# Optimization experiments

Measured on AMD Instinct MI355X. Metric: run time of the kernel, lower is better.

## Reference

```python
import jax, jax.numpy as jnp
import numpy as np

B, T_EN, T_DE, D_EN, D_DE, UNITS = 16, 256, 256, 512, 512, 128


def setup_inputs() -> dict:
    key = jax.random.key(0)
    k1, k2, k3, k4, k5 = jax.random.split(key, 5)
    # glorot-uniform style scale for weights
    def glorot(k, shape):
        lim = np.sqrt(6.0 / (shape[0] + shape[1]))
        return jax.random.uniform(k, shape, jnp.float32, -lim, lim)
    return {
        "en_seq": jax.random.normal(k1, (B, T_EN, D_EN), jnp.float32),
        "de_seq": jax.random.normal(k2, (B, T_DE, D_DE), jnp.float32),
        "w_en": glorot(k3, (D_EN, UNITS)),
        "w_de": glorot(k4, (D_DE, UNITS)),
        "nu": glorot(k5, (UNITS, 1)),
    }


def reference(en_seq, de_seq, w_en, w_de, nu):
    # Additive (Bahdanau) time attention.
    # Original keras code builds the (de, en) cross product via K.repeat /
    # K.repeat_elements with de-major, en-minor ordering; equivalent to
    # broadcasting att_de over a new en axis and att_en over a new de axis.
    att_en = jnp.einsum("bie,eu->biu", en_seq, w_en)   # (B, T_en, U)
    att_de = jnp.einsum("bjd,du->bju", de_seq, w_de)   # (B, T_de, U)
    # co_m: (B, T_de, T_en, U) — the large broadcast intermediate
    co_m = jnp.tanh(att_de[:, :, None, :] + att_en[:, None, :, :])
    mu = jnp.einsum("bjiu,u->bji", co_m, nu[:, 0])      # (B, T_de, T_en)
    alphas = jax.nn.softmax(mu, axis=-1)                # softmax over encoder time
    sum_en = jnp.einsum("bji,bie->bje", alphas, en_seq)  # (B, T_de, D_en)
    return jnp.concatenate([de_seq, sum_en], axis=-1)    # (B, T_de, D_de + D_en)
```

## Files before the change

kernel.cpp:

```cpp
#include <hip/hip_runtime.h>
#include <hip/hip_bf16.h>

#define TANH_SCALE 2.8853900817779268f

__global__ __launch_bounds__(256) void proj_kernel(
        const float* __restrict__ en, const float* __restrict__ de,
        const float* __restrict__ w_en, const float* __restrict__ w_de,
        float* __restrict__ Een, float* __restrict__ Ede) {
    const float* X;
    const float* W;
    float* OUT;
    if (blockIdx.y == 0) { X = en; W = w_en; OUT = Een; }
    else                 { X = de; W = w_de; OUT = Ede; }

    __shared__ float xt[64][36];
    __shared__ float wsh[64][128];
    const int tid  = threadIdx.x;
    const int tr   = tid >> 5;
    const int tc   = tid & 31;
    const int row0 = blockIdx.x * 32;

    const int xs_r  = tid >> 4;
    const int xs_k4 = (tid & 15) * 4;
    float4 xr[2], wr[8];

    auto g_load = [&](int kt) {
#pragma unroll
        for (int s = 0; s < 2; ++s) {
            int r = xs_r + 16 * s;
            xr[s] = *reinterpret_cast<const float4*>(
                X + (size_t)(row0 + r) * 512 + kt + xs_k4);
        }
#pragma unroll
        for (int s = 0; s < 8; ++s) {
            int idx = tid + 256 * s;
            int k = idx >> 5, c4 = (idx & 31) * 4;
            wr[s] = *reinterpret_cast<const float4*>(
                W + (size_t)(kt + k) * 128 + c4);
        }
    };
    auto lds_store = [&]() {
        const int swz = ((xs_k4 >> 2) & 7) << 2;
#pragma unroll
        for (int s = 0; s < 2; ++s) {
            int r = (xs_r + 16 * s) ^ swz;
            xt[xs_k4 + 0][r] = xr[s].x;
            xt[xs_k4 + 1][r] = xr[s].y;
            xt[xs_k4 + 2][r] = xr[s].z;
            xt[xs_k4 + 3][r] = xr[s].w;
        }
#pragma unroll
        for (int s = 0; s < 8; ++s) {
            int idx = tid + 256 * s;
            int k = idx >> 5, c4 = (idx & 31) * 4;
            *reinterpret_cast<float4*>(&wsh[k][c4]) = wr[s];
        }
    };

    float acc[4][4] = {{0.f}};
    g_load(0);
    lds_store();
    __syncthreads();

    for (int kt = 0; kt < 512; kt += 64) {
        const bool has_next = (kt + 64) < 512;
        if (has_next) g_load(kt + 64);
#pragma unroll
        for (int k = 0; k < 64; ++k) {
            const int col = (tr * 4) ^ (((k >> 2) & 7) << 2);
            float4 xv = *reinterpret_cast<const float4*>(&xt[k][col]);
            float4 wv = *reinterpret_cast<const float4*>(&wsh[k][tc * 4]);
            acc[0][0] = fmaf(xv.x, wv.x, acc[0][0]);
            acc[0][1] = fmaf(xv.x, wv.y, acc[0][1]);
            acc[0][2] = fmaf(xv.x, wv.z, acc[0][2]);
            acc[0][3] = fmaf(xv.x, wv.w, acc[0][3]);
            acc[1][0] = fmaf(xv.y, wv.x, acc[1][0]);
            acc[1][1] = fmaf(xv.y, wv.y, acc[1][1]);
            acc[1][2] = fmaf(xv.y, wv.z, acc[1][2]);
            acc[1][3] = fmaf(xv.y, wv.w, acc[1][3]);
            acc[2][0] = fmaf(xv.z, wv.x, acc[2][0]);
            acc[2][1] = fmaf(xv.z, wv.y, acc[2][1]);
            acc[2][2] = fmaf(xv.z, wv.z, acc[2][2]);
            acc[2][3] = fmaf(xv.z, wv.w, acc[2][3]);
            acc[3][0] = fmaf(xv.w, wv.x, acc[3][0]);
            acc[3][1] = fmaf(xv.w, wv.y, acc[3][1]);
            acc[3][2] = fmaf(xv.w, wv.z, acc[3][2]);
            acc[3][3] = fmaf(xv.w, wv.w, acc[3][3]);
        }
        __syncthreads();
        if (has_next) {
            lds_store();
            __syncthreads();
        }
    }

#pragma unroll
    for (int r = 0; r < 4; ++r) {
        float4 o;
        o.x = __builtin_exp2f(-TANH_SCALE * acc[r][0]);
        o.y = __builtin_exp2f(-TANH_SCALE * acc[r][1]);
        o.z = __builtin_exp2f(-TANH_SCALE * acc[r][2]);
        o.w = __builtin_exp2f(-TANH_SCALE * acc[r][3]);
        *reinterpret_cast<float4*>(
            OUT + (size_t)(row0 + tr * 4 + r) * 128 + tc * 4) = o;
    }
}

__global__ __launch_bounds__(512, 4) void fused_attn_kernel(
        const float* __restrict__ Een, const float* __restrict__ Ede,
        const float* __restrict__ nu, const float* __restrict__ en,
        const float* __restrict__ de, float* __restrict__ out) {
    const int phys = blockIdx.x;
    const int lid  = (phys & 7) * 64 + (phys >> 3);
    const int b    = lid >> 5;
    const int j0   = (lid & 31) * 8;
    const int tid  = threadIdx.x;
    const int i    = tid & 255;
    const int uh   = tid >> 8;

    __shared__ float ede_sh[8][128];
    __shared__ float nu2_sh[128];
    __shared__ float nusum_sh[64];
    __shared__ float al[8][256];
    __shared__ float red[8][4];

    if (tid < 256)
        reinterpret_cast<float4*>(&ede_sh[0][0])[tid] =
            reinterpret_cast<const float4*>(Ede + ((size_t)b * 256 + j0) * 128)[tid];
    if (tid >= 256 && tid < 384) nu2_sh[tid - 256] = 2.0f * nu[tid - 256];
    if (tid >= 384 && tid < 448) {
        int t = tid - 384;
        nusum_sh[t] = 2.0f * (nu[2 * t] + nu[2 * t + 1]);
    }

    {
        const float4* dsrc =
            reinterpret_cast<const float4*>(de + ((size_t)b * 256 + j0) * 512);
#pragma unroll
        for (int t = 0; t < 2; ++t) {
            int idx = tid + 512 * t;
            int j = idx >> 7, c4 = idx & 127;
            reinterpret_cast<float4*>(out + (size_t)(b * 256 + j0 + j) * 1024)[c4] =
                dsrc[idx];
        }
    }
    __syncthreads();

    float s[4] = {0.0f, 0.0f, 0.0f, 0.0f};
    const float4* e4 =
        reinterpret_cast<const float4*>(Een + ((size_t)b * 256 + i) * 128);
    const float4* nu4 = reinterpret_cast<const float4*>(nu2_sh);
    const float4* cs4 = reinterpret_cast<const float4*>(nusum_sh);
    for (int q = 0; q < 16; ++q) {
        const float4 ea = e4[2 * q];
        const float4 eb = e4[2 * q + 1];
        const float4 na = nu4[2 * q];
        const float4 nb = nu4[2 * q + 1];
        const float4 cs = cs4[q];
#pragma unroll
        for (int jl = 0; jl < 4; ++jl) {
            const float* dr = &ede_sh[uh * 4 + jl][8 * q];
            const float4 da = *reinterpret_cast<const float4*>(dr);
            const float4 db = *reinterpret_cast<const float4*>(dr + 4);
            float e0, e1, den, num;
            e0 = ea.x * da.x; e1 = ea.y * da.y;
            den = 1.0f + e0; den = fmaf(den, e1, den);
            num = fmaf(na.x, e1, cs.x); num = fmaf(na.y, e0, num);
            s[jl] = fmaf(num, __builtin_amdgcn_rcpf(den), s[jl]);
            e0 = ea.z * da.z; e1 = ea.w * da.w;
            den = 1.0f + e0; den = fmaf(den, e1, den);
            num = fmaf(na.z, e1, cs.y); num = fmaf(na.w, e0, num);
            s[jl] = fmaf(num, __builtin_amdgcn_rcpf(den), s[jl]);
            e0 = eb.x * db.x; e1 = eb.y * db.y;
            den = 1.0f + e0; den = fmaf(den, e1, den);
            num = fmaf(nb.x, e1, cs.z); num = fmaf(nb.y, e0, num);
            s[jl] = fmaf(num, __builtin_amdgcn_rcpf(den), s[jl]);
            e0 = eb.z * db.z; e1 = eb.w * db.w;
            den = 1.0f + e0; den = fmaf(den, e1, den);
            num = fmaf(nb.z, e1, cs.w); num = fmaf(nb.w, e0, num);
            s[jl] = fmaf(num, __builtin_amdgcn_rcpf(den), s[jl]);
        }
    }

    float p[4];
#pragma unroll
    for (int jl = 0; jl < 4; ++jl) p[jl] = __expf(s[jl]);
    const int lane = tid & 63;
    const int w    = (tid >> 6) & 3;
#pragma unroll
    for (int jl = 0; jl < 4; ++jl) {
        float t = p[jl];
#pragma unroll
        for (int off = 32; off >= 1; off >>= 1) t += __shfl_xor(t, off);
        if (lane == 0) red[uh * 4 + jl][w] = t;
    }
    __syncthreads();
#pragma unroll
    for (int jl = 0; jl < 4; ++jl) {
        const int j = uh * 4 + jl;
        float T = red[j][0] + red[j][1] + red[j][2] + red[j][3];
        al[j][i] = p[jl] * __builtin_amdgcn_rcpf(T);
    }
    __syncthreads();

    float acc[8];
#pragma unroll
    for (int j = 0; j < 8; ++j) acc[j] = 0.0f;
    const float* enb = en + (size_t)b * 256 * 512;
    const int c = tid;
    for (int i0 = 0; i0 < 256; i0 += 4) {
        float a[8][4];
#pragma unroll
        for (int j = 0; j < 8; ++j) {
            float4 v = *reinterpret_cast<const float4*>(&al[j][i0]);
            a[j][0] = v.x; a[j][1] = v.y; a[j][2] = v.z; a[j][3] = v.w;
        }
#pragma unroll
        for (int ii = 0; ii < 4; ++ii) {
            float e0 = enb[(size_t)(i0 + ii) * 512 + c];
#pragma unroll
            for (int j = 0; j < 8; ++j)
                acc[j] = fmaf(a[j][ii], e0, acc[j]);
        }
    }
#pragma unroll
    for (int j = 0; j < 8; ++j) {
        size_t row = (size_t)(b * 256 + j0 + j);
        out[row * 1024 + 512 + c] = acc[j];
    }
}

extern "C" void kernel_launch(void* const* d_in, const int* in_sizes, int n_in,
                              void* d_out, int out_size, void* d_ws, size_t ws_size,
                              hipStream_t stream) {
    const float* en   = (const float*)d_in[0];
    const float* de   = (const float*)d_in[1];
    const float* w_en = (const float*)d_in[2];
    const float* w_de = (const float*)d_in[3];
    const float* nu   = (const float*)d_in[4];
    float* out = (float*)d_out;

    char* ws = (char*)d_ws;
    float* Een = (float*)(ws);
    float* Ede = (float*)(ws + (size_t)4096 * 128 * 4);

    proj_kernel<<<dim3(128, 2), 256, 0, stream>>>(en, de, w_en, w_de, Een, Ede);
    fused_attn_kernel<<<dim3(512), 512, 0, stream>>>(Een, Ede, nu, en, de, out);
}
```

Measured before the change: 160.9 us.

## Split-K projection GEMM with combine pass and transposed encoder layout with prefetch

The projection GEMM can now be split along K into two halves, which doubles the block count. A separate combine kernel adds the partials and applies the exp2 transform, but only when the workspace is large enough. The encoder projection is written in a transposed, u-pair-major layout so that threads in the attention kernel read consecutive i values as coalesced float2 loads. The attention loop also register-prefetches the next group of encoder values. The trade-off is an extra kernel launch and extra partial-sum traffic in exchange for more parallelism in the small projection and better load coalescing in the main kernel.

```diff
diff --git a/kernel.cpp b/kernel.cpp
--- a/kernel.cpp
+++ b/kernel.cpp
@@ -3,40 +3,25 @@
 
 #define TANH_SCALE 2.8853900817779268f
 
-__global__ __launch_bounds__(256) void proj_kernel(
-        const float* __restrict__ en, const float* __restrict__ de,
-        const float* __restrict__ w_en, const float* __restrict__ w_de,
-        float* __restrict__ Een, float* __restrict__ Ede) {
-    const float* X;
-    const float* W;
-    float* OUT;
-    if (blockIdx.y == 0) { X = en; W = w_en; OUT = Een; }
-    else                 { X = de; W = w_de; OUT = Ede; }
-
-    __shared__ float xt[64][36];
-    __shared__ float wsh[64][128];
-    const int tid  = threadIdx.x;
-    const int tr   = tid >> 5;
-    const int tc   = tid & 31;
-    const int row0 = blockIdx.x * 32;
-
+
+__device__ __forceinline__ void gemm_tile_32x128(
+        const float* __restrict__ X, const float* __restrict__ W,
+        int row0, int k0, int k1, int tid, float acc[4][4],
+        float (*xt)[36], float (*wsh)[128]) {
     const int xs_r  = tid >> 4;
     const int xs_k4 = (tid & 15) * 4;
     float4 xr[2], wr[8];
 
     auto g_load = [&](int kt) {
 #pragma unroll
-        for (int s = 0; s < 2; ++s) {
-            int r = xs_r + 16 * s;
+        for (int s = 0; s < 2; ++s)
             xr[s] = *reinterpret_cast<const float4*>(
-                X + (size_t)(row0 + r) * 512 + kt + xs_k4);
-        }
+                X + (size_t)(row0 + xs_r + 16 * s) * 512 + kt + xs_k4);
 #pragma unroll
         for (int s = 0; s < 8; ++s) {
             int idx = tid + 256 * s;
-            int k = idx >> 5, c4 = (idx & 31) * 4;
             wr[s] = *reinterpret_cast<const float4*>(
-                W + (size_t)(kt + k) * 128 + c4);
+                W + (size_t)(kt + (idx >> 5)) * 128 + (idx & 31) * 4);
         }
     };
     auto lds_store = [&]() {
@@ -52,18 +37,16 @@
 #pragma unroll
         for (int s = 0; s < 8; ++s) {
             int idx = tid + 256 * s;
-            int k = idx >> 5, c4 = (idx & 31) * 4;
-            *reinterpret_cast<float4*>(&wsh[k][c4]) = wr[s];
+            *reinterpret_cast<float4*>(&wsh[idx >> 5][(idx & 31) * 4]) = wr[s];
         }
     };
 
-    float acc[4][4] = {{0.f}};
-    g_load(0);
+    const int tr = tid >> 5, tc = tid & 31;
+    g_load(k0);
     lds_store();
     __syncthreads();
-
-    for (int kt = 0; kt < 512; kt += 64) {
-        const bool has_next = (kt + 64) < 512;
+    for (int kt = k0; kt < k1; kt += 64) {
+        const bool has_next = (kt + 64) < k1;
         if (has_next) g_load(kt + 64);
 #pragma unroll
         for (int k = 0; k < 64; ++k) {
@@ -93,21 +76,101 @@
             __syncthreads();
         }
     }
-
-#pragma unroll
-    for (int r = 0; r < 4; ++r) {
-        float4 o;
-        o.x = __builtin_exp2f(-TANH_SCALE * acc[r][0]);
-        o.y = __builtin_exp2f(-TANH_SCALE * acc[r][1]);
-        o.z = __builtin_exp2f(-TANH_SCALE * acc[r][2]);
-        o.w = __builtin_exp2f(-TANH_SCALE * acc[r][3]);
-        *reinterpret_cast<float4*>(
-            OUT + (size_t)(row0 + tr * 4 + r) * 128 + tc * 4) = o;
+}
+
+__global__ __launch_bounds__(256) void proj_split_kernel(
+        const float* __restrict__ en, const float* __restrict__ de,
+        const float* __restrict__ w_en, const float* __restrict__ w_de,
+        float* __restrict__ P) {
+    __shared__ float xt[64][36];
+    __shared__ float wsh[64][128];
+    const bool is_en = (blockIdx.y == 0);
+    const float* X = is_en ? en : de;
+    const float* W = is_en ? w_en : w_de;
+    const int row0 = blockIdx.x * 32;
+    const int kq   = blockIdx.z;
+
+    float acc[4][4] = {{0.f}};
+    gemm_tile_32x128(X, W, row0, kq * 256, kq * 256 + 256, threadIdx.x,
+                     acc, xt, wsh);
+
+    float* OUT = P + (size_t)(blockIdx.y * 2 + kq) * 524288;
+    const int tr = threadIdx.x >> 5, tc = threadIdx.x & 31;
+#pragma unroll
+    for (int r = 0; r < 4; ++r)
+        *reinterpret_cast<float4*>(OUT + (size_t)(row0 + tr * 4 + r) * 128 + tc * 4)
+            = make_float4(acc[r][0], acc[r][1], acc[r][2], acc[r][3]);
+}
+
+__global__ __launch_bounds__(256) void combine_kernel(
+        const float* __restrict__ P, float* __restrict__ Ete,
+        float* __restrict__ Ede) {
+    const int gid = blockIdx.x * 256 + threadIdx.x;
+    const float* Pm = P + (size_t)blockIdx.y * 1048576;
+    float4 a = reinterpret_cast<const float4*>(Pm)[gid];
+    float4 b = reinterpret_cast<const float4*>(Pm + 524288)[gid];
+    float4 v;
+    v.x = __builtin_exp2f(-TANH_SCALE * (a.x + b.x));
+    v.y = __builtin_exp2f(-TANH_SCALE * (a.y + b.y));
+    v.z = __builtin_exp2f(-TANH_SCALE * (a.z + b.z));
+    v.w = __builtin_exp2f(-TANH_SCALE * (a.w + b.w));
+    if (blockIdx.y == 1) {
+        reinterpret_cast<float4*>(Ede)[gid] = v;
+    } else {
+        const int row = gid >> 5, u4 = gid & 31;
+        const int b_ = row >> 8, i = row & 255;
+        float* base = Ete + (size_t)b_ * 32768 + (size_t)(u4 * 2) * 512 + i * 2;
+        *reinterpret_cast<float2*>(base)       = make_float2(v.x, v.y);
+        *reinterpret_cast<float2*>(base + 512) = make_float2(v.z, v.w);
+    }
+}
+
+__global__ __launch_bounds__(256) void proj_full_kernel(
+        const float* __restrict__ en, const float* __restrict__ de,
+        const float* __restrict__ w_en, const float* __restrict__ w_de,
+        float* __restrict__ Ete, float* __restrict__ Ede) {
+    __shared__ float xt[64][36];
+    __shared__ float wsh[64][128];
+    const bool is_en = (blockIdx.y == 0);
+    const float* X = is_en ? en : de;
+    const float* W = is_en ? w_en : w_de;
+    const int row0 = blockIdx.x * 32;
+
+    float acc[4][4] = {{0.f}};
+    gemm_tile_32x128(X, W, row0, 0, 512, threadIdx.x, acc, xt, wsh);
+
+    const int tr = threadIdx.x >> 5, tc = threadIdx.x & 31;
+    float v[4][4];
+#pragma unroll
+    for (int r = 0; r < 4; ++r)
+#pragma unroll
+        for (int c = 0; c < 4; ++c)
+            v[r][c] = __builtin_exp2f(-TANH_SCALE * acc[r][c]);
+
+    if (!is_en) {
+#pragma unroll
+        for (int r = 0; r < 4; ++r)
+            *reinterpret_cast<float4*>(
+                Ede + (size_t)(row0 + tr * 4 + r) * 128 + tc * 4) =
+                make_float4(v[r][0], v[r][1], v[r][2], v[r][3]);
+    } else {
+        const int b_ = row0 >> 8;
+        const int il0 = (row0 & 255) + tr * 4;
+#pragma unroll
+        for (int cp = 0; cp < 2; ++cp) {
+            size_t base = (size_t)b_ * 32768 + (size_t)(tc * 2 + cp) * 512 + il0 * 2;
+            *reinterpret_cast<float4*>(Ete + base) =
+                make_float4(v[0][2 * cp], v[0][2 * cp + 1],
+                            v[1][2 * cp], v[1][2 * cp + 1]);
+            *reinterpret_cast<float4*>(Ete + base + 4) =
+                make_float4(v[2][2 * cp], v[2][2 * cp + 1],
+                            v[3][2 * cp], v[3][2 * cp + 1]);
+        }
     }
 }
 
 __global__ __launch_bounds__(512, 4) void fused_attn_kernel(
-        const float* __restrict__ Een, const float* __restrict__ Ede,
+        const float* __restrict__ Ete, const float* __restrict__ Ede,
         const float* __restrict__ nu, const float* __restrict__ en,
         const float* __restrict__ de, float* __restrict__ out) {
     const int phys = blockIdx.x;
@@ -147,13 +210,19 @@
     __syncthreads();
 
     float s[4] = {0.0f, 0.0f, 0.0f, 0.0f};
-    const float4* e4 =
-        reinterpret_cast<const float4*>(Een + ((size_t)b * 256 + i) * 128);
+    const float2* ep =
+        reinterpret_cast<const float2*>(Ete) + (size_t)b * 16384 + i;
     const float4* nu4 = reinterpret_cast<const float4*>(nu2_sh);
     const float4* cs4 = reinterpret_cast<const float4*>(nusum_sh);
+
+    float2 evc[4], evn[4];
+#pragma unroll
+    for (int t = 0; t < 4; ++t) evc[t] = ep[t * 256];
     for (int q = 0; q < 16; ++q) {
-        const float4 ea = e4[2 * q];
-        const float4 eb = e4[2 * q + 1];
+        if (q < 15) {
+#pragma unroll
+            for (int t = 0; t < 4; ++t) evn[t] = ep[(4 * (q + 1) + t) * 256];
+        }
         const float4 na = nu4[2 * q];
         const float4 nb = nu4[2 * q + 1];
         const float4 cs = cs4[q];
@@ -163,22 +232,26 @@
             const float4 da = *reinterpret_cast<const float4*>(dr);
             const float4 db = *reinterpret_cast<const float4*>(dr + 4);
             float e0, e1, den, num;
-            e0 = ea.x * da.x; e1 = ea.y * da.y;
+            e0 = evc[0].x * da.x; e1 = evc[0].y * da.y;
             den = 1.0f + e0; den = fmaf(den, e1, den);
             num = fmaf(na.x, e1, cs.x); num = fmaf(na.y, e0, num);
             s[jl] = fmaf(num, __builtin_amdgcn_rcpf(den), s[jl]);
-            e0 = ea.z * da.z; e1 = ea.w * da.w;
+            e0 = evc[1].x * da.z; e1 = evc[1].y * da.w;
             den = 1.0f + e0; den = fmaf(den, e1, den);
             num = fmaf(na.z, e1, cs.y); num = fmaf(na.w, e0, num);
             s[jl] = fmaf(num, __builtin_amdgcn_rcpf(den), s[jl]);
-            e0 = eb.x * db.x; e1 = eb.y * db.y;
+            e0 = evc[2].x * db.x; e1 = evc[2].y * db.y;
             den = 1.0f + e0; den = fmaf(den, e1, den);
             num = fmaf(nb.x, e1, cs.z); num = fmaf(nb.y, e0, num);
             s[jl] = fmaf(num, __builtin_amdgcn_rcpf(den), s[jl]);
-            e0 = eb.z * db.z; e1 = eb.w * db.w;
+            e0 = evc[3].x * db.z; e1 = evc[3].y * db.w;
             den = 1.0f + e0; den = fmaf(den, e1, den);
             num = fmaf(nb.z, e1, cs.w); num = fmaf(nb.w, e0, num);
             s[jl] = fmaf(num, __builtin_amdgcn_rcpf(den), s[jl]);
+        }
+        if (q < 15) {
+#pragma unroll
+            for (int t = 0; t < 4; ++t) evc[t] = evn[t];
         }
     }
 
@@ -241,9 +314,18 @@
     float* out = (float*)d_out;
 
     char* ws = (char*)d_ws;
-    float* Een = (float*)(ws);
-    float* Ede = (float*)(ws + (size_t)4096 * 128 * 4);
-
-    proj_kernel<<<dim3(128, 2), 256, 0, stream>>>(en, de, w_en, w_de, Een, Ede);
-    fused_attn_kernel<<<dim3(512), 512, 0, stream>>>(Een, Ede, nu, en, de, out);
-}
+    float* Ete = (float*)(ws);
+    float* Ede = (float*)(ws + (size_t)2 * 1024 * 1024);
+    float* P   = (float*)(ws + (size_t)4 * 1024 * 1024);
+
+    const bool split = ws_size >= (size_t)12 * 1024 * 1024;
+    if (split) {
+        proj_split_kernel<<<dim3(128, 2, 2), 256, 0, stream>>>(
+            en, de, w_en, w_de, P);
+        combine_kernel<<<dim3(512, 2), 256, 0, stream>>>(P, Ete, Ede);
+    } else {
+        proj_full_kernel<<<dim3(128, 2), 256, 0, stream>>>(
+            en, de, w_en, w_de, Ete, Ede);
+    }
+    fused_attn_kernel<<<dim3(512), 512, 0, stream>>>(Ete, Ede, nu, en, de, out);
+}
```

After: 162.1 us. About the same (+0.7%).
